# Kernel tuning notes

Measured on AMD Instinct MI355X. Metric: run time of the kernel, lower is better.

## Reference

```python
import jax, jax.numpy as jnp
import numpy as np

B, L1, L, DIM_IN, DIM_H, DIM_M = 8, 64, 1024, 512, 512, 512


def setup_inputs() -> dict:
    key = jax.random.key(0)
    ks = jax.random.split(key, 7)
    return {
        "query": jax.random.normal(ks[0], (L1, DIM_H), dtype=jnp.float32),
        "keys": jax.random.normal(ks[1], (B, L, DIM_IN), dtype=jnp.float32),
        "values": jax.random.normal(ks[2], (B, L, DIM_IN), dtype=jnp.float32),
        # nn.Linear weights: Wx (dim_middle, dim_in) no bias; Wh (dim_middle, dim_h) with bias; w (dim_middle,) no bias
        "Wx": jax.random.normal(ks[3], (DIM_M, DIM_IN), dtype=jnp.float32) * 0.02,
        "Wh": jax.random.normal(ks[4], (DIM_M, DIM_H), dtype=jnp.float32) * 0.02,
        "bh": jax.random.normal(ks[5], (DIM_M,), dtype=jnp.float32) * 0.02,
        "w": jax.random.normal(ks[6], (DIM_M,), dtype=jnp.float32) * 0.02,
    }


def reference(query, keys, values, Wx, Wh, bh, w):
    # mode='concept': query [l1, dh], keys/values [b, l, d]
    kx = jnp.einsum('bld,md->blm', keys, Wx)          # [b, l, m]
    qh = jnp.einsum('qd,md->qm', query, Wh) + bh       # [l1, m]
    g = jax.nn.relu(kx[:, None, :, :] + qh[None, :, None, :])  # [b, l1, l, m]
    scores = jnp.einsum('bqlm,m->bql', g, w)           # [b, l1, l]
    e = jax.nn.softmax(scores, axis=-1)                # softmax over key len (dim 2)
    return jnp.einsum('bql,bld->bqd', e, values)       # [b, l1, dv]
```

## Files before the change

kernel.cpp:

```cpp
#include <hip/hip_runtime.h>
#include <hip/hip_bf16.h>

#define BB 8
#define L1 64
#define LL 1024
#define DD 512

typedef float f32x4 __attribute__((ext_vector_type(4)));
typedef _Float16 f16;
typedef _Float16 f16x2 __attribute__((ext_vector_type(2)));
typedef _Float16 f16x4 __attribute__((ext_vector_type(4)));
typedef _Float16 f16x8 __attribute__((ext_vector_type(8)));

union F16x8u { f16x8 v; f16x2 h[4]; };
union U4H8 { uint4 u; f16x8 v; };

__global__ __launch_bounds__(256) void kxqh_kernel(
    const float* __restrict__ keys,
    const float* __restrict__ query,
    const float* __restrict__ Wx,
    const float* __restrict__ Wh,
    const float* __restrict__ bh,
    f16* __restrict__ kx,
    f16* __restrict__ qh) {
  __shared__ char lds[32768] __attribute__((aligned(128)));
  const int t = threadIdx.x;
  const int lane = t & 63;
  const int w = t >> 6;
  const int fq = lane >> 4, fr = lane & 15;
  const int bid = blockIdx.x;

  if (bid < 8) {
    const int m0 = bid * 64;
    const int wid = w;
    f32x4 acc[4] = {};
    float4 rq[4], rw[4];
#define LOADQ(KC)                                                              \
    do {                                                                       \
      _Pragma("unroll") for (int i = 0; i < 4; ++i) {                          \
        int slot = t + i * 256;                                                \
        int row = slot >> 4, c4 = (slot & 15) * 4;                             \
        rq[i] = *reinterpret_cast<const float4*>(query + (size_t)row * DD + (KC)*64 + c4); \
        rw[i] = *reinterpret_cast<const float4*>(Wh + (size_t)(m0 + row) * DD + (KC)*64 + c4); \
      }                                                                        \
    } while (0)
    LOADQ(0);
    for (int kc = 0; kc < 8; ++kc) {
      #pragma unroll
      for (int i = 0; i < 4; ++i) {
        int slot = t + i * 256;
        int row = slot >> 4, c4 = (slot & 15) * 4;
        f16x4 hq, hw;
        hq[0] = (f16)rq[i].x; hq[1] = (f16)rq[i].y; hq[2] = (f16)rq[i].z; hq[3] = (f16)rq[i].w;
        hw[0] = (f16)rw[i].x; hw[1] = (f16)rw[i].y; hw[2] = (f16)rw[i].z; hw[3] = (f16)rw[i].w;
        *reinterpret_cast<f16x4*>(lds + row * 144 + c4 * 2) = hq;
        *reinterpret_cast<f16x4*>(lds + 9216 + row * 144 + c4 * 2) = hw;
      }
      if (kc < 7) LOADQ(kc + 1);
      __syncthreads();
      #pragma unroll
      for (int kh = 0; kh < 2; ++kh) {
        f16x8 bf = *reinterpret_cast<const f16x8*>(
            lds + 9216 + (wid * 16 + fr) * 144 + kh * 64 + fq * 16);
        #pragma unroll
        for (int qf = 0; qf < 4; ++qf) {
          f16x8 af = *reinterpret_cast<const f16x8*>(
              lds + (qf * 16 + fr) * 144 + kh * 64 + fq * 16);
          acc[qf] = __builtin_amdgcn_mfma_f32_16x16x32_f16(af, bf, acc[qf], 0, 0, 0);
        }
      }
      __syncthreads();
    }
#undef LOADQ
    #pragma unroll
    for (int qf = 0; qf < 4; ++qf) {
      int m = m0 + wid * 16 + fr;
      float bias = bh[m];
      #pragma unroll
      for (int r = 0; r < 4; ++r)
        qh[(size_t)(qf * 16 + fq * 4 + r) * DD + m] = (f16)(acc[qf][r] + bias);
    }
    return;
  }

  const int kb = bid - 8;
  const int rt = kb & 127;
  const int mt = kb >> 7;
  const int rowA0 = rt * 64;
  const int m0 = mt * 64;
  const int wr = w >> 1, wc = w & 1;

  f32x4 acc[2][2] = {};
  float4 ra[4], rb[4];

#define LOADK(K0)                                                              \
  do {                                                                         \
    _Pragma("unroll") for (int i = 0; i < 4; ++i) {                            \
      int flat = t * 4 + i * 1024;                                             \
      int row = flat >> 6, col = flat & 63;                                    \
      ra[i] = *reinterpret_cast<const float4*>(keys + (size_t)(rowA0 + row) * DD + (K0) + col); \
      rb[i] = *reinterpret_cast<const float4*>(Wx + (size_t)(m0 + row) * DD + (K0) + col); \
    }                                                                          \
  } while (0)

  LOADK(0);
  for (int s = 0; s < 8; ++s) {
    const int base = (s & 1) * 16384;
    #pragma unroll
    for (int i = 0; i < 4; ++i) {
      int flat = t * 4 + i * 1024;
      int row = flat >> 6, col = flat & 63;
      f16x4 ha, hb;
      ha[0] = (f16)ra[i].x; ha[1] = (f16)ra[i].y; ha[2] = (f16)ra[i].z; ha[3] = (f16)ra[i].w;
      hb[0] = (f16)rb[i].x; hb[1] = (f16)rb[i].y; hb[2] = (f16)rb[i].z; hb[3] = (f16)rb[i].w;
      int byte = row * 128 + ((col * 2) ^ ((row & 7) << 4));
      *reinterpret_cast<f16x4*>(lds + base + byte) = ha;
      *reinterpret_cast<f16x4*>(lds + base + 8192 + byte) = hb;
    }
    if (s < 7) LOADK((s + 1) * 64);
    __syncthreads();
    #pragma unroll
    for (int kh = 0; kh < 2; ++kh) {
      f16x8 af[2], bf[2];
      #pragma unroll
      for (int mi = 0; mi < 2; ++mi) {
        int row = wr * 32 + mi * 16 + fr;
        af[mi] = *reinterpret_cast<const f16x8*>(
            lds + base + row * 128 + ((kh * 64 + fq * 16) ^ ((row & 7) << 4)));
      }
      #pragma unroll
      for (int ni = 0; ni < 2; ++ni) {
        int row = wc * 32 + ni * 16 + fr;
        bf[ni] = *reinterpret_cast<const f16x8*>(
            lds + base + 8192 + row * 128 + ((kh * 64 + fq * 16) ^ ((row & 7) << 4)));
      }
      #pragma unroll
      for (int mi = 0; mi < 2; ++mi)
        #pragma unroll
        for (int ni = 0; ni < 2; ++ni)
          acc[mi][ni] = __builtin_amdgcn_mfma_f32_16x16x32_f16(
              af[mi], bf[ni], acc[mi][ni], 0, 0, 0);
    }
  }
#undef LOADK
  #pragma unroll
  for (int mi = 0; mi < 2; ++mi) {
    #pragma unroll
    for (int ni = 0; ni < 2; ++ni) {
      int row = rowA0 + wr * 32 + mi * 16 + fq * 4;
      int col = m0 + wc * 32 + ni * 16 + fr;
      #pragma unroll
      for (int r = 0; r < 4; ++r)
        kx[(size_t)(row + r) * DD + col] = (f16)acc[mi][ni][r];
    }
  }
}

__global__ __launch_bounds__(512) void score6_kernel(
    const f16* __restrict__ kx,
    const f16* __restrict__ qh,
    const float* __restrict__ w,
    f16* __restrict__ sc,
    float* __restrict__ pmax) {
  const int b = blockIdx.x & 7;
  const int l0 = (blockIdx.x >> 3) * 32;
  const int t = threadIdx.x;
  __shared__ __align__(16) char kxs[32 * 256];
  __shared__ __align__(16) char qhs[64 * 256];
  __shared__ __align__(16) f16 wsf[DD];
  __shared__ float smax[64][17];
  if (t < 128) {
    float4 wv = *reinterpret_cast<const float4*>(w + t * 4);
    f16x4 hv; hv[0] = (f16)wv.x; hv[1] = (f16)wv.y; hv[2] = (f16)wv.z; hv[3] = (f16)wv.w;
    *reinterpret_cast<f16x4*>(&wsf[t * 4]) = hv;
  }
  const int qb = t & 31;
  const int lp = t >> 5;
  float acc[2][2] = {};
  uint4 rkx, rqh[2];

#define LOADM(M0)                                                              \
  do {                                                                         \
    {                                                                          \
      int row = t >> 4, col = (t & 15) * 8;                                    \
      rkx = *reinterpret_cast<const uint4*>(kx + (size_t)(b * LL + l0 + row) * DD + (M0) + col); \
    }                                                                          \
    _Pragma("unroll") for (int p = 0; p < 2; ++p) {                            \
      int slot = t + p * 512;                                                  \
      int row = slot >> 4, col = (slot & 15) * 8;                              \
      rqh[p] = *reinterpret_cast<const uint4*>(qh + (size_t)row * DD + (M0) + col); \
    }                                                                          \
  } while (0)

  LOADM(0);
  for (int m0 = 0; m0 < DD; m0 += 128) {
    {
      int row = t >> 4, cb = (t & 15) * 16;
      *reinterpret_cast<uint4*>(kxs + row * 256 + (cb ^ ((row & 7) << 4))) = rkx;
    }
    #pragma unroll
    for (int p = 0; p < 2; ++p) {
      int slot = t + p * 512;
      int row = slot >> 4, cb = (slot & 15) * 16;
      *reinterpret_cast<uint4*>(qhs + row * 256 + (cb ^ ((row & 15) << 4))) = rqh[p];
    }
    if (m0 < DD - 128) LOADM(m0 + 128);
    __syncthreads();
    #pragma unroll 2
    for (int mm = 0; mm < 128; mm += 8) {
      const int mb = mm * 2;
      F16x8u kv0, kv1, wv;
      {
        int r0 = lp * 2, r1 = lp * 2 + 1;
        kv0.v = *reinterpret_cast<const f16x8*>(kxs + r0 * 256 + (mb ^ ((r0 & 7) << 4)));
        kv1.v = *reinterpret_cast<const f16x8*>(kxs + r1 * 256 + (mb ^ ((r1 & 7) << 4)));
      }
      wv.v = *reinterpret_cast<const f16x8*>(&wsf[m0 + mm]);
      #pragma unroll
      for (int j = 0; j < 2; ++j) {
        int qr = qb + 32 * j;
        F16x8u qv, g0, g1;
        qv.v = *reinterpret_cast<const f16x8*>(qhs + qr * 256 + (mb ^ ((qr & 15) << 4)));
        f16x8 zz = {};
        g0.v = __builtin_elementwise_max(kv0.v + qv.v, zz);
        g1.v = __builtin_elementwise_max(kv1.v + qv.v, zz);
        #pragma unroll
        for (int c = 0; c < 4; ++c) {
          acc[0][j] = __builtin_amdgcn_fdot2(g0.h[c], wv.h[c], acc[0][j], false);
          acc[1][j] = __builtin_amdgcn_fdot2(g1.h[c], wv.h[c], acc[1][j], false);
        }
      }
    }
    __syncthreads();
  }
#undef LOADM
  #pragma unroll
  for (int i = 0; i < 2; ++i)
    #pragma unroll
    for (int j = 0; j < 2; ++j)
      sc[((size_t)b * L1 + qb + 32 * j) * LL + l0 + lp * 2 + i] = (f16)acc[i][j];
  #pragma unroll
  for (int j = 0; j < 2; ++j)
    smax[qb + 32 * j][lp] = fmaxf(acc[0][j], acc[1][j]);
  __syncthreads();
  if (t < 64) {
    float m = smax[t][0];
    #pragma unroll
    for (int i = 1; i < 16; ++i) m = fmaxf(m, smax[t][i]);
    pmax[((size_t)b * L1 + t) * 32 + (l0 >> 5)] = m;
  }
}

__global__ __launch_bounds__(512) void fso3_kernel(
    const f16* __restrict__ sc,
    const float* __restrict__ pmax,
    const float* __restrict__ v,
    float* __restrict__ out) {
  __shared__ __align__(16) char es[64 * 256];
  __shared__ __align__(16) char vt[16 * 256];
  __shared__ float rowm[64];
  __shared__ float rowinv[64];
  __shared__ float spart[64][17];
  __shared__ f32x4 accbuf[4][64];
  const int t = threadIdx.x;
  const int lane = t & 63;
  const int w = t >> 6;
  const int fq = lane >> 4, fr = lane & 15;
  const int bid = blockIdx.x;
  const int b = bid & 7;
  const int d0 = (bid >> 3) * 16;
  const f16* scb = sc + (size_t)b * L1 * LL;
  const float* vb = v + (size_t)b * LL * DD;

  const int r0 = t >> 4;
  const int r1 = (t + 512) >> 4;
  const int ec8 = t & 15;
  const int vl = t >> 2;
  const int dq = (t & 3) * 4;
  uint4 rsc[2];
  float4 rv;

#define LOADC(LC)                                                              \
  do {                                                                         \
    rsc[0] = *reinterpret_cast<const uint4*>(scb + (size_t)r0 * LL + (LC) * 128 + ec8 * 8); \
    rsc[1] = *reinterpret_cast<const uint4*>(scb + (size_t)r1 * LL + (LC) * 128 + ec8 * 8); \
    rv = *reinterpret_cast<const float4*>(                                     \
        vb + (size_t)((LC) * 128 + vl) * DD + d0 + dq);                        \
  } while (0)

  LOADC(0);
  if (t < 64) {
    const float* pm = pmax + ((size_t)b * L1 + t) * 32;
    float4 m4 = *reinterpret_cast<const float4*>(pm);
    #pragma unroll
    for (int i = 1; i < 8; ++i) {
      float4 x = *reinterpret_cast<const float4*>(pm + i * 4);
      m4.x = fmaxf(m4.x, x.x); m4.y = fmaxf(m4.y, x.y);
      m4.z = fmaxf(m4.z, x.z); m4.w = fmaxf(m4.w, x.w);
    }
    rowm[t] = fmaxf(fmaxf(m4.x, m4.y), fmaxf(m4.z, m4.w));
  }
  __syncthreads();
  float rmv[2] = {rowm[r0], rowm[r1]};
  float spp[2] = {0.f, 0.f};
  f32x4 acc = {};
  const int qs = (w & 3) * 16;
  const int ksh = (w >> 2) * 2;

  for (int c = 0; c < 8; ++c) {
    #pragma unroll
    for (int p = 0; p < 2; ++p) {
      int q = p ? r1 : r0;
      U4H8 x; x.u = rsc[p];
      f16x8 h;
      #pragma unroll
      for (int j = 0; j < 8; ++j) {
        float e = __expf((float)x.v[j] - rmv[p]);
        spp[p] += e;
        h[j] = (f16)e;
      }
      int byte = q * 256 + ((ec8 * 16) ^ ((q & 7) << 4));
      *reinterpret_cast<f16x8*>(es + byte) = h;
    }
    {
      float vs[4] = {rv.x, rv.y, rv.z, rv.w};
      #pragma unroll
      for (int j = 0; j < 4; ++j) {
        int d = dq + j;
        int byte = d * 256 + ((2 * vl) ^ ((d & 7) << 4));
        *reinterpret_cast<f16*>(vt + byte) = (f16)vs[j];
      }
    }
    if (c < 7) LOADC(c + 1);
    __syncthreads();
    #pragma unroll
    for (int ki = 0; ki < 2; ++ki) {
      int ks = ksh + ki;
      int qa = qs + fr;
      int colb = ks * 64 + fq * 16;
      f16x8 a = *reinterpret_cast<const f16x8*>(es + qa * 256 + (colb ^ ((qa & 7) << 4)));
      f16x8 bb = *reinterpret_cast<const f16x8*>(vt + fr * 256 + (colb ^ ((fr & 7) << 4)));
      acc = __builtin_amdgcn_mfma_f32_16x16x32_f16(a, bb, acc, 0, 0, 0);
    }
    __syncthreads();
  }
#undef LOADC
  spart[r0][ec8] = spp[0];
  spart[r1][ec8] = spp[1];
  if (w >= 4) accbuf[w & 3][lane] = acc;
  __syncthreads();
  if (t < 64) {
    float S = 0.f;
    #pragma unroll
    for (int i = 0; i < 16; ++i) S += spart[t][i];
    rowinv[t] = 1.f / S;
  }
  __syncthreads();
  if (w < 4) {
    f32x4 ah = accbuf[w][lane];
    acc += ah;
    #pragma unroll
    for (int r = 0; r < 4; ++r) {
      int q = qs + fq * 4 + r;
      out[((size_t)b * L1 + q) * DD + d0 + fr] = acc[r] * rowinv[q];
    }
  }
}

extern "C" void kernel_launch(void* const* d_in, const int* in_sizes, int n_in,
                              void* d_out, int out_size, void* d_ws, size_t ws_size,
                              hipStream_t stream) {
  const float* query  = (const float*)d_in[0];
  const float* keys   = (const float*)d_in[1];
  const float* values = (const float*)d_in[2];
  const float* Wx     = (const float*)d_in[3];
  const float* Wh     = (const float*)d_in[4];
  const float* bh     = (const float*)d_in[5];
  const float* w      = (const float*)d_in[6];
  float* out = (float*)d_out;

  char* ws = (char*)d_ws;
  f16*   kx   = (f16*)ws;
  f16*   qh   = (f16*)(ws + 8388608);
  f16*   sc   = (f16*)(ws + 8454144);
  float* pmax = (float*)(ws + 9502720);

  kxqh_kernel<<<1032, 256, 0, stream>>>(keys, query, Wx, Wh, bh, kx, qh);
  score6_kernel<<<256, 512, 0, stream>>>(kx, qh, w, sc, pmax);
  fso3_kernel<<<256, 512, 0, stream>>>(sc, pmax, values, out);
}
```

Baseline: 48.00 us.

## Retile score kernel to 64x32 l-by-q tiles with 4x2 register blocking

The score kernel now runs 256 threads per block, each owning a 64-key by 32-query tile, with every thread computing a 4x2 register block instead of 2x2. Each loaded key and query fragment is reused across more outputs, which cuts LDS reads per FLOP, and the LDS swizzles are changed to match the new access pattern. Per-tile partial maxima are split into two 32-wide halves so the pmax layout stays the same. The cost is fewer threads per block, more registers per thread, and possible occupancy loss.

```diff
diff --git a/kernel.cpp b/kernel.cpp
--- a/kernel.cpp
+++ b/kernel.cpp
@@ -156,78 +156,89 @@
   }
 }
 
-__global__ __launch_bounds__(512) void score6_kernel(
+__global__ __launch_bounds__(256) void score10_kernel(
     const f16* __restrict__ kx,
     const f16* __restrict__ qh,
     const float* __restrict__ w,
     f16* __restrict__ sc,
     float* __restrict__ pmax) {
-  const int b = blockIdx.x & 7;
-  const int l0 = (blockIdx.x >> 3) * 32;
+  const int bid = blockIdx.x;
+  const int b = bid & 7;
+  const int lt = (bid >> 3) & 15;
+  const int l0 = lt * 64;
+  const int q0 = (bid >> 7) * 32;
   const int t = threadIdx.x;
-  __shared__ __align__(16) char kxs[32 * 256];
-  __shared__ __align__(16) char qhs[64 * 256];
+  __shared__ __align__(16) char kxs[64 * 256];
+  __shared__ __align__(16) char qhs[32 * 256];
   __shared__ __align__(16) f16 wsf[DD];
-  __shared__ float smax[64][17];
+  __shared__ float smax[32][17];
   if (t < 128) {
     float4 wv = *reinterpret_cast<const float4*>(w + t * 4);
     f16x4 hv; hv[0] = (f16)wv.x; hv[1] = (f16)wv.y; hv[2] = (f16)wv.z; hv[3] = (f16)wv.w;
     *reinterpret_cast<f16x4*>(&wsf[t * 4]) = hv;
   }
-  const int qb = t & 31;
-  const int lp = t >> 5;
-  float acc[2][2] = {};
-  uint4 rkx, rqh[2];
+  const int lg = t & 15;
+  const int qg = t >> 4;
+  float acc[4][2] = {};
+  uint4 rkx[4], rqh[2];
 
 #define LOADM(M0)                                                              \
   do {                                                                         \
-    {                                                                          \
-      int row = t >> 4, col = (t & 15) * 8;                                    \
-      rkx = *reinterpret_cast<const uint4*>(kx + (size_t)(b * LL + l0 + row) * DD + (M0) + col); \
+    _Pragma("unroll") for (int p = 0; p < 4; ++p) {                            \
+      int slot = t + p * 256;                                                  \
+      int row = slot >> 4, col = (slot & 15) * 8;                              \
+      rkx[p] = *reinterpret_cast<const uint4*>(kx + (size_t)(b * LL + l0 + row) * DD + (M0) + col); \
     }                                                                          \
     _Pragma("unroll") for (int p = 0; p < 2; ++p) {                            \
-      int slot = t + p * 512;                                                  \
+      int slot = t + p * 256;                                                  \
       int row = slot >> 4, col = (slot & 15) * 8;                              \
-      rqh[p] = *reinterpret_cast<const uint4*>(qh + (size_t)row * DD + (M0) + col); \
+      rqh[p] = *reinterpret_cast<const uint4*>(qh + (size_t)(q0 + row) * DD + (M0) + col); \
     }                                                                          \
   } while (0)
 
   LOADM(0);
   for (int m0 = 0; m0 < DD; m0 += 128) {
-    {
-      int row = t >> 4, cb = (t & 15) * 16;
-      *reinterpret_cast<uint4*>(kxs + row * 256 + (cb ^ ((row & 7) << 4))) = rkx;
+    #pragma unroll
+    for (int p = 0; p < 4; ++p) {
+      int slot = t + p * 256;
+      int row = slot >> 4, cb = (slot & 15) * 16;
+      *reinterpret_cast<uint4*>(kxs + row * 256 + (cb ^ (((row >> 2) & 15) << 4))) = rkx[p];
     }
     #pragma unroll
     for (int p = 0; p < 2; ++p) {
-      int slot = t + p * 512;
+      int slot = t + p * 256;
       int row = slot >> 4, cb = (slot & 15) * 16;
-      *reinterpret_cast<uint4*>(qhs + row * 256 + (cb ^ ((row & 15) << 4))) = rqh[p];
+      *reinterpret_cast<uint4*>(qhs + row * 256 + (cb ^ (((row >> 1) & 15) << 4))) = rqh[p];
     }
     if (m0 < DD - 128) LOADM(m0 + 128);
     __syncthreads();
     #pragma unroll 2
     for (int mm = 0; mm < 128; mm += 8) {
       const int mb = mm * 2;
-      F16x8u kv0, kv1, wv;
-      {
-        int r0 = lp * 2, r1 = lp * 2 + 1;
-        kv0.v = *reinterpret_cast<const f16x8*>(kxs + r0 * 256 + (mb ^ ((r0 & 7) << 4)));
-        kv1.v = *reinterpret_cast<const f16x8*>(kxs + r1 * 256 + (mb ^ ((r1 & 7) << 4)));
+      F16x8u kv[4], wv, qv[2];
+      #pragma unroll
+      for (int i = 0; i < 4; ++i) {
+        int row = lg * 4 + i;
+        kv[i].v = *reinterpret_cast<const f16x8*>(
+            kxs + row * 256 + (mb ^ (((row >> 2) & 15) << 4)));
       }
       wv.v = *reinterpret_cast<const f16x8*>(&wsf[m0 + mm]);
       #pragma unroll
       for (int j = 0; j < 2; ++j) {
-        int qr = qb + 32 * j;
-        F16x8u qv, g0, g1;
-        qv.v = *reinterpret_cast<const f16x8*>(qhs + qr * 256 + (mb ^ ((qr & 15) << 4)));
-        f16x8 zz = {};
-        g0.v = __builtin_elementwise_max(kv0.v + qv.v, zz);
-        g1.v = __builtin_elementwise_max(kv1.v + qv.v, zz);
+        int row = qg * 2 + j;
+        qv[j].v = *reinterpret_cast<const f16x8*>(
+            qhs + row * 256 + (mb ^ (((row >> 1) & 15) << 4)));
+      }
+      #pragma unroll
+      for (int i = 0; i < 4; ++i) {
         #pragma unroll
-        for (int c = 0; c < 4; ++c) {
-          acc[0][j] = __builtin_amdgcn_fdot2(g0.h[c], wv.h[c], acc[0][j], false);
-          acc[1][j] = __builtin_amdgcn_fdot2(g1.h[c], wv.h[c], acc[1][j], false);
+        for (int j = 0; j < 2; ++j) {
+          f16x8 zz = {};
+          F16x8u g;
+          g.v = __builtin_elementwise_max(kv[i].v + qv[j].v, zz);
+          #pragma unroll
+          for (int c = 0; c < 4; ++c)
+            acc[i][j] = __builtin_amdgcn_fdot2(g.h[c], wv.h[c], acc[i][j], false);
         }
       }
     }
@@ -235,19 +246,22 @@
   }
 #undef LOADM
   #pragma unroll
-  for (int i = 0; i < 2; ++i)
+  for (int i = 0; i < 4; ++i)
     #pragma unroll
     for (int j = 0; j < 2; ++j)
-      sc[((size_t)b * L1 + qb + 32 * j) * LL + l0 + lp * 2 + i] = (f16)acc[i][j];
+      sc[((size_t)b * L1 + q0 + qg * 2 + j) * LL + l0 + lg * 4 + i] = (f16)acc[i][j];
   #pragma unroll
-  for (int j = 0; j < 2; ++j)
-    smax[qb + 32 * j][lp] = fmaxf(acc[0][j], acc[1][j]);
+  for (int j = 0; j < 2; ++j) {
+    float m = fmaxf(fmaxf(acc[0][j], acc[1][j]), fmaxf(acc[2][j], acc[3][j]));
+    smax[qg * 2 + j][lg] = m;
+  }
   __syncthreads();
   if (t < 64) {
-    float m = smax[t][0];
-    #pragma unroll
-    for (int i = 1; i < 16; ++i) m = fmaxf(m, smax[t][i]);
-    pmax[((size_t)b * L1 + t) * 32 + (l0 >> 5)] = m;
+    int qr = t >> 1, half = t & 1;
+    float m = smax[qr][half * 8];
+    #pragma unroll
+    for (int i = 1; i < 8; ++i) m = fmaxf(m, smax[qr][half * 8 + i]);
+    pmax[((size_t)b * L1 + q0 + qr) * 32 + lt * 2 + half] = m;
   }
 }
 
@@ -386,6 +400,6 @@
   float* pmax = (float*)(ws + 9502720);
 
   kxqh_kernel<<<1032, 256, 0, stream>>>(keys, query, Wx, Wh, bh, kx, qh);
-  score6_kernel<<<256, 512, 0, stream>>>(kx, qh, w, sc, pmax);
+  score10_kernel<<<256, 256, 0, stream>>>(kx, qh, w, sc, pmax);
   fso3_kernel<<<256, 512, 0, stream>>>(sc, pmax, values, out);
 }
```

Result: slower. 51.35 us (+7.0%).
